# Optimization experiments

Hardware: AMD Instinct MI355X
Metric: run time of the kernel (lower is better)

The kernel has to match this reference:

```python
import jax, jax.numpy as jnp
import numpy as np

B, S, HID, NH = 8, 384, 512, 8
HD = HID // NH
SCALE = float(np.sqrt(HID))  # torch code scales by sqrt(full hidden_units), not head dim
EPS = 1e-6


def setup_inputs() -> dict:
    key = jax.random.key(0)
    ks = jax.random.split(key, 6)
    enc = jax.random.normal(ks[0], (B, S, HID), jnp.float32)
    # mask: (B,1,S,S); fill=ones, made causal (lower-triangular) so masking is exercised
    mask = jnp.broadcast_to(jnp.tril(jnp.ones((S, S), jnp.int32)), (B, 1, S, S))
    init = 1.0 / np.sqrt(HID)
    Wq = jax.random.normal(ks[1], (HID, HID), jnp.float32) * init
    Wk = jax.random.normal(ks[2], (HID, HID), jnp.float32) * init
    Wv = jax.random.normal(ks[3], (HID, HID), jnp.float32) * init
    Wo = jax.random.normal(ks[4], (HID, HID), jnp.float32) * init
    ln_gamma = jnp.ones((HID,), jnp.float32)
    ln_beta = jnp.zeros((HID,), jnp.float32)
    return {"enc": enc, "mask": mask, "Wq": Wq, "Wk": Wk, "Wv": Wv, "Wo": Wo,
            "ln_gamma": ln_gamma, "ln_beta": ln_beta}


def reference(enc, mask, Wq, Wk, Wv, Wo, ln_gamma, ln_beta):
    # enc: (B,S,HID); torch Linear(no bias): y = x @ W.T
    def heads(x, W):
        return (x @ W.T).reshape(B, S, NH, HD).transpose(0, 2, 1, 3)  # (B,H,S,D)

    q, k, v = heads(enc, Wq), heads(enc, Wk), heads(enc, Wv)
    # intersample scores: query (b,h,q) vs key (c,h,k) -> (B,H,C,Sq,Sk)
    scores = jnp.einsum('bhqd,chkd->bhcqk', q, k) / SCALE
    m = mask[:, 0]  # (C,S,S): key-sample mask
    scores = jnp.where(m[None, None] == 0, -1.0e9, scores)
    # joint softmax over (key-sample c, key-position k)
    sw = scores.transpose(0, 1, 3, 2, 4).reshape(B, NH, S, B * S)
    w = jax.nn.softmax(sw, axis=-1).reshape(B, NH, S, B, S).transpose(0, 1, 3, 2, 4)  # (B,H,C,Sq,Sk)
    ctx = jnp.einsum('bhcqk,chkd->bhqd', w, v)            # (B,H,S,D)
    ctx = ctx.transpose(0, 2, 1, 3).reshape(B, S, HID)     # (B,S,HID)
    out = ctx @ Wo.T + enc                                 # W_O + residual (dropout=identity, eval)
    mu = out.mean(-1, keepdims=True)
    var = ((out - mu) ** 2).mean(-1, keepdims=True)
    out = (out - mu) / jnp.sqrt(var + EPS) * ln_gamma + ln_beta
    return (out, w)
```

## Files before the change

kernel.cpp:

```cpp
#include <hip/hip_runtime.h>
#include <hip/hip_bf16.h>

#define B_    8
#define S_    384
#define HID_  512
#define NH_   8
#define HD_   64
#define T_    3072
static constexpr float INV_SCALE = 0.044194173824159216f;

typedef float  f32x4  __attribute__((ext_vector_type(4)));
typedef __bf16 bf16x8 __attribute__((ext_vector_type(8)));
typedef __bf16 bf16x4 __attribute__((ext_vector_type(4)));

#define MFMA(a, b, c) __builtin_amdgcn_mfma_f32_16x16x32_bf16((a), (b), (c), 0, 0, 0)

__global__ __launch_bounds__(256)
void cvt_kernel(const float* __restrict__ enc, const float* __restrict__ Wq,
                const float* __restrict__ Wk,  const float* __restrict__ Wv,
                const float* __restrict__ Wo,
                __bf16* __restrict__ encB, __bf16* __restrict__ WqB,
                __bf16* __restrict__ WkB,  __bf16* __restrict__ WvB,
                __bf16* __restrict__ WoB)
{
    const int E  = T_ * HID_ / 4;
    const int W4 = HID_ * HID_ / 4;
    int i = blockIdx.x * 256 + threadIdx.x;
    const float* src; __bf16* dst; int off;
    if      (i < E)          { src = enc; dst = encB; off = i; }
    else if (i < E + W4)     { src = Wq;  dst = WqB;  off = i - E; }
    else if (i < E + 2 * W4) { src = Wk;  dst = WkB;  off = i - E - W4; }
    else if (i < E + 3 * W4) { src = Wv;  dst = WvB;  off = i - E - 2 * W4; }
    else                     { src = Wo;  dst = WoB;  off = i - E - 3 * W4; }
    f32x4 v = *(const f32x4*)(src + (size_t)off * 4);
    bf16x4 o;
    #pragma unroll
    for (int j = 0; j < 4; ++j) o[j] = (__bf16)v[j];
    *(bf16x4*)(dst + (size_t)off * 4) = o;
}

__global__ __launch_bounds__(256)
void qkv_kernel(const __bf16* __restrict__ enc,
                const __bf16* __restrict__ Wq,
                const __bf16* __restrict__ Wk,
                const __bf16* __restrict__ Wv,
                __bf16* __restrict__ Qs,
                __bf16* __restrict__ Ks,
                __bf16* __restrict__ Vt)
{
    const int w    = threadIdx.x >> 6;
    const int lane = threadIdx.x & 63;
    const int col  = lane & 15;
    const int quad = lane >> 4;
    const int m0   = blockIdx.x * 64 + w * 16;
    const int n0   = blockIdx.y * 64;
    const int z    = blockIdx.z;
    const __bf16* W = (z == 0) ? Wq : (z == 1) ? Wk : Wv;

    f32x4 acc[4];
    #pragma unroll
    for (int j = 0; j < 4; ++j) acc[j] = (f32x4){0.f, 0.f, 0.f, 0.f};

    const __bf16* arow = enc + (size_t)(m0 + col) * HID_;
    for (int k0 = 0; k0 < HID_; k0 += 32) {
        bf16x8 a = *(const bf16x8*)(arow + k0 + quad * 8);
        #pragma unroll
        for (int j = 0; j < 4; ++j) {
            bf16x8 b = *(const bf16x8*)(W + (size_t)(n0 + j * 16 + col) * HID_ + k0 + quad * 8);
            acc[j] = MFMA(a, b, acc[j]);
        }
    }

    if (z == 2) {
        #pragma unroll
        for (int j = 0; j < 4; ++j) {
            int n = n0 + j * 16 + col;
            bf16x4 pk;
            #pragma unroll
            for (int r = 0; r < 4; ++r) pk[r] = (__bf16)acc[j][r];
            *(bf16x4*)(Vt + (size_t)n * T_ + m0 + quad * 4) = pk;
        }
    } else {
        __bf16* Oo = (z == 0) ? Qs : Ks;
        float sc = (z == 0) ? INV_SCALE : 1.0f;
        #pragma unroll
        for (int j = 0; j < 4; ++j)
            #pragma unroll
            for (int r = 0; r < 4; ++r)
                Oo[(size_t)(m0 + quad * 4 + r) * HID_ + n0 + j * 16 + col] =
                    (__bf16)(acc[j][r] * sc);
    }
}

__global__ __launch_bounds__(512)
void attn_core(const __bf16* __restrict__ Qs,
               const __bf16* __restrict__ Ks,
               const __bf16* __restrict__ Vt,
               __bf16* __restrict__ ctxB,
               float* __restrict__ rlws)
{
    const int qt   = blockIdx.x;
    const int h    = blockIdx.y;
    const int b    = blockIdx.z;
    const int tid  = threadIdx.x;
    const int W    = tid >> 6;
    const int half = W >> 2;
    const int w    = W & 3;
    const int lane = tid & 63;
    const int col  = lane & 15;
    const int quad = lane >> 4;

    __shared__ __bf16 elds[8][16][72];
    __shared__ float  cred[4][16][68];
    __shared__ float  lred[4][16][16];

    const int qq_base = w * 16 + quad * 4;

    const __bf16* qrow = Qs + (size_t)(b * S_ + qt * 64 + w * 16 + col) * HID_ + h * HD_;
    bf16x8 aQ0 = *(const bf16x8*)(qrow + quad * 8);
    bf16x8 aQ1 = *(const bf16x8*)(qrow + 32 + quad * 8);

    f32x4 acc[4];
    #pragma unroll
    for (int j = 0; j < 4; ++j) acc[j] = (f32x4){0.f, 0.f, 0.f, 0.f};
    float lp[4] = {0.f, 0.f, 0.f, 0.f};

    const int NC = B_ * (qt + 1);
    for (int idx = half; idx < NC; idx += 2) {
        const int c  = idx / (qt + 1);
        const int kc = idx % (qt + 1);
        const int kt0 = c * S_ + kc * 64;
        const bool diag = (kc == qt);
        #pragma unroll
        for (int nt = 0; nt < 4; ++nt) {
            const __bf16* krow = Ks + (size_t)(kt0 + nt * 16 + col) * HID_ + h * HD_;
            bf16x8 bK0 = *(const bf16x8*)(krow + quad * 8);
            bf16x8 bK1 = *(const bf16x8*)(krow + 32 + quad * 8);
            f32x4 s = (f32x4){0.f, 0.f, 0.f, 0.f};
            s = MFMA(aQ0, bK0, s);
            s = MFMA(aQ1, bK1, s);
            const int kk = nt * 16 + col;
            #pragma unroll
            for (int r = 0; r < 4; ++r) {
                float e = (!diag || kk <= qq_base + r) ? __expf(s[r]) : 0.f;
                lp[r] += e;
                elds[W][quad * 4 + r][kk] = (__bf16)e;
            }
        }
        #pragma unroll
        for (int ks = 0; ks < 2; ++ks) {
            bf16x8 aE = *(const bf16x8*)(&elds[W][col][ks * 32 + quad * 8]);
            #pragma unroll
            for (int nt = 0; nt < 4; ++nt) {
                bf16x8 bV = *(const bf16x8*)(Vt + (size_t)(h * HD_ + nt * 16 + col) * T_ +
                                             kt0 + ks * 32 + quad * 8);
                acc[nt] = MFMA(aE, bV, acc[nt]);
            }
        }
    }

    if (half == 1) {
        #pragma unroll
        for (int nt = 0; nt < 4; ++nt)
            #pragma unroll
            for (int r = 0; r < 4; ++r)
                cred[w][quad * 4 + r][nt * 16 + col] = acc[nt][r];
        #pragma unroll
        for (int r = 0; r < 4; ++r)
            lred[w][quad * 4 + r][col] = lp[r];
    }
    __syncthreads();
    if (half == 1) return;

    #pragma unroll
    for (int r = 0; r < 4; ++r)
        lp[r] += lred[w][quad * 4 + r][col];
    #pragma unroll
    for (int nt = 0; nt < 4; ++nt)
        #pragma unroll
        for (int r = 0; r < 4; ++r)
            acc[nt][r] += cred[w][quad * 4 + r][nt * 16 + col];

    float rl[4];
    #pragma unroll
    for (int r = 0; r < 4; ++r) {
        float v = lp[r];
        v += __shfl_xor(v, 1);
        v += __shfl_xor(v, 2);
        v += __shfl_xor(v, 4);
        v += __shfl_xor(v, 8);
        rl[r] = 1.0f / v;
    }
    if (col == 0) {
        #pragma unroll
        for (int r = 0; r < 4; ++r)
            rlws[(size_t)(b * NH_ + h) * S_ + qt * 64 + qq_base + r] = rl[r];
    }

    #pragma unroll
    for (int nt = 0; nt < 4; ++nt)
        #pragma unroll
        for (int r = 0; r < 4; ++r)
            ctxB[(size_t)(b * S_ + qt * 64 + qq_base + r) * HID_ + h * HD_ + nt * 16 + col] =
                (__bf16)(acc[nt][r] * rl[r]);
}

__global__ __launch_bounds__(256)
void tail_kernel(const __bf16* __restrict__ Qs,
                 const __bf16* __restrict__ Ks,
                 const float* __restrict__ rlws,
                 float* __restrict__ wout,
                 const __bf16* __restrict__ ctxB,
                 const __bf16* __restrict__ WoB,
                 const float* __restrict__ enc,
                 const float* __restrict__ gamma,
                 const float* __restrict__ beta,
                 float* __restrict__ out)
{
    const int tid  = threadIdx.x;
    const int w    = tid >> 6;
    const int lane = tid & 63;
    const int col  = lane & 15;
    const int quad = lane >> 4;

    __shared__ float elds[4][16][68];
    __shared__ float s_sums[16][4][2];

    if (blockIdx.x < 3) {
        const int t0 = ((blockIdx.x * NH_ + blockIdx.y) * B_ + blockIdx.z) * 16;
        const int wv = w;

        f32x4 acc[8];
        #pragma unroll
        for (int nt = 0; nt < 8; ++nt) acc[nt] = (f32x4){0.f, 0.f, 0.f, 0.f};

        const __bf16* arow = ctxB + (size_t)(t0 + col) * HID_;
        for (int step = 0; step < 16; ++step) {
            bf16x8 a = *(const bf16x8*)(arow + step * 32 + quad * 8);
            #pragma unroll
            for (int nt = 0; nt < 8; ++nt) {
                bf16x8 bW = *(const bf16x8*)(WoB + (size_t)(wv * 128 + nt * 16 + col) * HID_ +
                                             step * 32 + quad * 8);
                acc[nt] = MFMA(a, bW, acc[nt]);
            }
        }

        const int trow = t0 + quad * 4;
        float psum[4] = {0.f, 0.f, 0.f, 0.f};
        float psq[4]  = {0.f, 0.f, 0.f, 0.f};
        #pragma unroll
        for (int nt = 0; nt < 8; ++nt) {
            int n = wv * 128 + nt * 16 + col;
            #pragma unroll
            for (int r = 0; r < 4; ++r) {
                float x = acc[nt][r] + enc[(size_t)(trow + r) * HID_ + n];
                acc[nt][r] = x;
                psum[r] += x;
                psq[r]  += x * x;
            }
        }
        #pragma unroll
        for (int r = 0; r < 4; ++r) {
            float v = psum[r], q2 = psq[r];
            v  += __shfl_xor(v, 1);  v  += __shfl_xor(v, 2);
            v  += __shfl_xor(v, 4);  v  += __shfl_xor(v, 8);
            q2 += __shfl_xor(q2, 1); q2 += __shfl_xor(q2, 2);
            q2 += __shfl_xor(q2, 4); q2 += __shfl_xor(q2, 8);
            if (col == 0) {
                s_sums[quad * 4 + r][wv][0] = v;
                s_sums[quad * 4 + r][wv][1] = q2;
            }
        }
        __syncthreads();

        #pragma unroll
        for (int r = 0; r < 4; ++r) {
            float sm = s_sums[quad * 4 + r][0][0] + s_sums[quad * 4 + r][1][0] +
                       s_sums[quad * 4 + r][2][0] + s_sums[quad * 4 + r][3][0];
            float sq = s_sums[quad * 4 + r][0][1] + s_sums[quad * 4 + r][1][1] +
                       s_sums[quad * 4 + r][2][1] + s_sums[quad * 4 + r][3][1];
            float mu   = sm * (1.0f / 512.0f);
            float var  = sq * (1.0f / 512.0f) - mu * mu;
            float rstd = rsqrtf(var + 1e-6f);
            #pragma unroll
            for (int nt = 0; nt < 8; ++nt) {
                int n = wv * 128 + nt * 16 + col;
                float y = (acc[nt][r] - mu) * rstd * gamma[n] + beta[n];
                out[(size_t)(trow + r) * HID_ + n] = y;
            }
        }
        return;
    }

    const int x    = blockIdx.x - 3;
    const int qt   = x % 6;
    const int c    = x / 6;
    const int h    = blockIdx.y;
    const int b    = blockIdx.z;
    const int wr   = lane >> 2;
    const int seg  = lane & 3;

    const int qq_base = w * 16 + quad * 4;

    const __bf16* qrow = Qs + (size_t)(b * S_ + qt * 64 + w * 16 + col) * HID_ + h * HD_;
    bf16x8 aQ0 = *(const bf16x8*)(qrow + quad * 8);
    bf16x8 aQ1 = *(const bf16x8*)(qrow + 32 + quad * 8);

    float rlv[4];
    #pragma unroll
    for (int r = 0; r < 4; ++r)
        rlv[r] = rlws[(size_t)(b * NH_ + h) * S_ + qt * 64 + qq_base + r];

    float* gb = wout + ((((size_t)(b * NH_ + h) * B_ + c) * S_ + qt * 64 + w * 16 + wr) * S_);

    for (int kc = 0; kc < 6; ++kc) {
        float* gp = gb + kc * 64 + seg * 16;
        if (kc > qt) {
            #pragma unroll
            for (int j = 0; j < 4; ++j)
                *(f32x4*)(gp + j * 4) = (f32x4){0.f, 0.f, 0.f, 0.f};
            continue;
        }
        const int kt0 = c * S_ + kc * 64;
        const bool diag = (kc == qt);
        #pragma unroll
        for (int nt = 0; nt < 4; ++nt) {
            const __bf16* krow = Ks + (size_t)(kt0 + nt * 16 + col) * HID_ + h * HD_;
            bf16x8 bK0 = *(const bf16x8*)(krow + quad * 8);
            bf16x8 bK1 = *(const bf16x8*)(krow + 32 + quad * 8);
            f32x4 s = (f32x4){0.f, 0.f, 0.f, 0.f};
            s = MFMA(aQ0, bK0, s);
            s = MFMA(aQ1, bK1, s);
            const int kk = nt * 16 + col;
            #pragma unroll
            for (int r = 0; r < 4; ++r) {
                float e = (!diag || kk <= qq_base + r) ? __expf(s[r]) * rlv[r] : 0.f;
                elds[w][quad * 4 + r][kk] = e;
            }
        }
        #pragma unroll
        for (int j = 0; j < 4; ++j)
            *(f32x4*)(gp + j * 4) = *(const f32x4*)(&elds[w][wr][seg * 16 + j * 4]);
    }
}

extern "C" void kernel_launch(void* const* d_in, const int* in_sizes, int n_in,
                              void* d_out, int out_size, void* d_ws, size_t ws_size,
                              hipStream_t stream)
{
    const float* enc   = (const float*)d_in[0];
    const float* Wq    = (const float*)d_in[2];
    const float* Wk    = (const float*)d_in[3];
    const float* Wv    = (const float*)d_in[4];
    const float* Wo    = (const float*)d_in[5];
    const float* gamma = (const float*)d_in[6];
    const float* beta  = (const float*)d_in[7];

    float* out  = (float*)d_out;
    float* wout = out + (size_t)T_ * HID_;

    char* ws = (char*)d_ws;
    const size_t SZ_TOK = (size_t)T_ * HID_ * sizeof(__bf16);
    const size_t SZ_W   = (size_t)HID_ * HID_ * sizeof(__bf16);
    __bf16* encB = (__bf16*)(ws);
    __bf16* WqB  = (__bf16*)(ws + SZ_TOK);
    __bf16* WkB  = (__bf16*)(ws + SZ_TOK + SZ_W);
    __bf16* WvB  = (__bf16*)(ws + SZ_TOK + 2 * SZ_W);
    __bf16* WoB  = (__bf16*)(ws + SZ_TOK + 3 * SZ_W);
    __bf16* Qs   = (__bf16*)(ws + SZ_TOK + 4 * SZ_W);
    __bf16* Ks   = (__bf16*)(ws + 2 * SZ_TOK + 4 * SZ_W);
    __bf16* Vt   = (__bf16*)(ws + 3 * SZ_TOK + 4 * SZ_W);
    __bf16* ctxB = (__bf16*)(ws + 4 * SZ_TOK + 4 * SZ_W);
    float*  rlws = (float*)(ws);

    cvt_kernel<<<dim3(2560), 256, 0, stream>>>(enc, Wq, Wk, Wv, Wo,
                                               encB, WqB, WkB, WvB, WoB);
    qkv_kernel<<<dim3(48, 8, 3), 256, 0, stream>>>(encB, WqB, WkB, WvB, Qs, Ks, Vt);
    attn_core<<<dim3(6, NH_, B_), 512, 0, stream>>>(Qs, Ks, Vt, ctxB, rlws);
    tail_kernel<<<dim3(51, NH_, B_), 256, 0, stream>>>(Qs, Ks, rlws, wout,
                                                       ctxB, WoB, enc, gamma, beta, out);
}
```

Baseline: 601.7 us.

## Fuse all stages into one cooperative persistent kernel with grid syncs

Merges the conversion, QKV projection, attention core and tail (weights output plus output projection and layernorm) into a single cooperative kernel of 256 blocks, with grid-wide syncs between stages. Work units are distributed over the persistent blocks in strided loops. This removes the gaps between kernel launches and the launch overhead, at the cost of grid-sync latency and a fixed block count that may balance poorly across stages. The original multi-kernel path stays as a fallback when cooperative launch is unavailable.

```diff
diff --git a/kernel.cpp b/kernel.cpp
--- a/kernel.cpp
+++ b/kernel.cpp
@@ -1,5 +1,8 @@
 #include <hip/hip_runtime.h>
+#include <hip/hip_cooperative_groups.h>
 #include <hip/hip_bf16.h>
+
+namespace cg = cooperative_groups;
 
 #define B_    8
 #define S_    384
@@ -14,6 +17,347 @@
 typedef __bf16 bf16x4 __attribute__((ext_vector_type(4)));
 
 #define MFMA(a, b, c) __builtin_amdgcn_mfma_f32_16x16x32_bf16((a), (b), (c), 0, 0, 0)
+
+#define NBLK 256
+#define NTHR 512
+
+__global__ __launch_bounds__(512, 2)
+void mega_kernel(const float* __restrict__ enc,
+                 const float* __restrict__ Wq,  const float* __restrict__ Wk,
+                 const float* __restrict__ Wv,  const float* __restrict__ Wo,
+                 const float* __restrict__ gamma, const float* __restrict__ beta,
+                 __bf16* __restrict__ encB, __bf16* __restrict__ WqB,
+                 __bf16* __restrict__ WkB,  __bf16* __restrict__ WvB,
+                 __bf16* __restrict__ WoB,
+                 __bf16* __restrict__ Qs,   __bf16* __restrict__ Ks,
+                 __bf16* __restrict__ Vt,   __bf16* __restrict__ ctxB,
+                 float* __restrict__ rlws,  float* __restrict__ wout,
+                 float* __restrict__ out)
+{
+    cg::grid_group grid = cg::this_grid();
+    const int blk = blockIdx.x;
+    const int tid = threadIdx.x;
+
+    __shared__ __align__(16) char smem[39936];
+
+    {
+        const int E  = T_ * HID_ / 4;
+        const int W4 = HID_ * HID_ / 4;
+        const int TOT = E + 4 * W4;
+        for (int i = blk * NTHR + tid; i < TOT; i += NBLK * NTHR) {
+            const float* src; __bf16* dst; int off;
+            if      (i < E)          { src = enc; dst = encB; off = i; }
+            else if (i < E + W4)     { src = Wq;  dst = WqB;  off = i - E; }
+            else if (i < E + 2 * W4) { src = Wk;  dst = WkB;  off = i - E - W4; }
+            else if (i < E + 3 * W4) { src = Wv;  dst = WvB;  off = i - E - 2 * W4; }
+            else                     { src = Wo;  dst = WoB;  off = i - E - 3 * W4; }
+            f32x4 v = *(const f32x4*)(src + (size_t)off * 4);
+            bf16x4 o;
+            #pragma unroll
+            for (int j = 0; j < 4; ++j) o[j] = (__bf16)v[j];
+            *(bf16x4*)(dst + (size_t)off * 4) = o;
+        }
+    }
+    grid.sync();
+
+    {
+        const int half = tid >> 8;
+        const int t2   = tid & 255;
+        const int w    = t2 >> 6;
+        const int lane = t2 & 63;
+        const int col  = lane & 15;
+        const int quad = lane >> 4;
+        for (int u = blk; u < 576; u += NBLK) {
+            const int vb = u * 2 + half;
+            const int x  = vb % 48;
+            const int y  = (vb / 48) % 8;
+            const int z  = vb / 384;
+            const int m0 = x * 64 + w * 16;
+            const int n0 = y * 64;
+            const __bf16* W = (z == 0) ? WqB : (z == 1) ? WkB : WvB;
+
+            f32x4 acc[4];
+            #pragma unroll
+            for (int j = 0; j < 4; ++j) acc[j] = (f32x4){0.f, 0.f, 0.f, 0.f};
+
+            const __bf16* arow = encB + (size_t)(m0 + col) * HID_;
+            for (int k0 = 0; k0 < HID_; k0 += 32) {
+                bf16x8 a = *(const bf16x8*)(arow + k0 + quad * 8);
+                #pragma unroll
+                for (int j = 0; j < 4; ++j) {
+                    bf16x8 b = *(const bf16x8*)(W + (size_t)(n0 + j * 16 + col) * HID_ + k0 + quad * 8);
+                    acc[j] = MFMA(a, b, acc[j]);
+                }
+            }
+
+            if (z == 2) {
+                #pragma unroll
+                for (int j = 0; j < 4; ++j) {
+                    int n = n0 + j * 16 + col;
+                    bf16x4 pk;
+                    #pragma unroll
+                    for (int r = 0; r < 4; ++r) pk[r] = (__bf16)acc[j][r];
+                    *(bf16x4*)(Vt + (size_t)n * T_ + m0 + quad * 4) = pk;
+                }
+            } else {
+                __bf16* Oo = (z == 0) ? Qs : Ks;
+                float sc = (z == 0) ? INV_SCALE : 1.0f;
+                #pragma unroll
+                for (int j = 0; j < 4; ++j)
+                    #pragma unroll
+                    for (int r = 0; r < 4; ++r)
+                        Oo[(size_t)(m0 + quad * 4 + r) * HID_ + n0 + j * 16 + col] =
+                            (__bf16)(acc[j][r] * sc);
+            }
+        }
+    }
+    grid.sync();
+
+    {
+        const int W    = tid >> 6;
+        const int half = W >> 2;
+        const int w    = W & 3;
+        const int lane = tid & 63;
+        const int col  = lane & 15;
+        const int quad = lane >> 4;
+
+        __bf16 (*elds)[16][72] = (__bf16(*)[16][72])(smem);
+        float  (*cred)[16][68] = (float(*)[16][68])(smem + 18432);
+        float  (*lred)[16][16] = (float(*)[16][16])(smem + 35840);
+
+        const int qq_base = w * 16 + quad * 4;
+
+        for (int u = blk; u < 384; u += NBLK) {
+            const int qt = u % 6;
+            const int h  = (u / 6) % 8;
+            const int b  = u / 48;
+
+            const __bf16* qrow = Qs + (size_t)(b * S_ + qt * 64 + w * 16 + col) * HID_ + h * HD_;
+            bf16x8 aQ0 = *(const bf16x8*)(qrow + quad * 8);
+            bf16x8 aQ1 = *(const bf16x8*)(qrow + 32 + quad * 8);
+
+            f32x4 acc[4];
+            #pragma unroll
+            for (int j = 0; j < 4; ++j) acc[j] = (f32x4){0.f, 0.f, 0.f, 0.f};
+            float lp[4] = {0.f, 0.f, 0.f, 0.f};
+
+            const int NC = B_ * (qt + 1);
+            for (int idx = half; idx < NC; idx += 2) {
+                const int c  = idx / (qt + 1);
+                const int kc = idx % (qt + 1);
+                const int kt0 = c * S_ + kc * 64;
+                const bool diag = (kc == qt);
+                #pragma unroll
+                for (int nt = 0; nt < 4; ++nt) {
+                    const __bf16* krow = Ks + (size_t)(kt0 + nt * 16 + col) * HID_ + h * HD_;
+                    bf16x8 bK0 = *(const bf16x8*)(krow + quad * 8);
+                    bf16x8 bK1 = *(const bf16x8*)(krow + 32 + quad * 8);
+                    f32x4 s = (f32x4){0.f, 0.f, 0.f, 0.f};
+                    s = MFMA(aQ0, bK0, s);
+                    s = MFMA(aQ1, bK1, s);
+                    const int kk = nt * 16 + col;
+                    #pragma unroll
+                    for (int r = 0; r < 4; ++r) {
+                        float e = (!diag || kk <= qq_base + r) ? __expf(s[r]) : 0.f;
+                        lp[r] += e;
+                        elds[W][quad * 4 + r][kk] = (__bf16)e;
+                    }
+                }
+                #pragma unroll
+                for (int ks = 0; ks < 2; ++ks) {
+                    bf16x8 aE = *(const bf16x8*)(&elds[W][col][ks * 32 + quad * 8]);
+                    #pragma unroll
+                    for (int nt = 0; nt < 4; ++nt) {
+                        bf16x8 bV = *(const bf16x8*)(Vt + (size_t)(h * HD_ + nt * 16 + col) * T_ +
+                                                     kt0 + ks * 32 + quad * 8);
+                        acc[nt] = MFMA(aE, bV, acc[nt]);
+                    }
+                }
+            }
+
+            if (half == 1) {
+                #pragma unroll
+                for (int nt = 0; nt < 4; ++nt)
+                    #pragma unroll
+                    for (int r = 0; r < 4; ++r)
+                        cred[w][quad * 4 + r][nt * 16 + col] = acc[nt][r];
+                #pragma unroll
+                for (int r = 0; r < 4; ++r)
+                    lred[w][quad * 4 + r][col] = lp[r];
+            }
+            __syncthreads();
+            if (half == 0) {
+                #pragma unroll
+                for (int r = 0; r < 4; ++r)
+                    lp[r] += lred[w][quad * 4 + r][col];
+                #pragma unroll
+                for (int nt = 0; nt < 4; ++nt)
+                    #pragma unroll
+                    for (int r = 0; r < 4; ++r)
+                        acc[nt][r] += cred[w][quad * 4 + r][nt * 16 + col];
+
+                float rl[4];
+                #pragma unroll
+                for (int r = 0; r < 4; ++r) {
+                    float v = lp[r];
+                    v += __shfl_xor(v, 1);
+                    v += __shfl_xor(v, 2);
+                    v += __shfl_xor(v, 4);
+                    v += __shfl_xor(v, 8);
+                    rl[r] = 1.0f / v;
+                }
+                if (col == 0) {
+                    #pragma unroll
+                    for (int r = 0; r < 4; ++r)
+                        rlws[(size_t)(b * NH_ + h) * S_ + qt * 64 + qq_base + r] = rl[r];
+                }
+                #pragma unroll
+                for (int nt = 0; nt < 4; ++nt)
+                    #pragma unroll
+                    for (int r = 0; r < 4; ++r)
+                        ctxB[(size_t)(b * S_ + qt * 64 + qq_base + r) * HID_ + h * HD_ + nt * 16 + col] =
+                            (__bf16)(acc[nt][r] * rl[r]);
+            }
+            __syncthreads();
+        }
+    }
+    grid.sync();
+
+    {
+        for (int u = blk; u < 1728; u += NBLK) {
+            if (u < 192) {
+                const int t0   = u * 16;
+                const int wv   = tid >> 6;
+                const int lane = tid & 63;
+                const int col  = lane & 15;
+                const int quad = lane >> 4;
+                float (*s_sums)[8][2] = (float(*)[8][2])(smem + 34816);
+
+                f32x4 acc[4];
+                #pragma unroll
+                for (int nt = 0; nt < 4; ++nt) acc[nt] = (f32x4){0.f, 0.f, 0.f, 0.f};
+
+                const __bf16* arow = ctxB + (size_t)(t0 + col) * HID_;
+                for (int step = 0; step < 16; ++step) {
+                    bf16x8 a = *(const bf16x8*)(arow + step * 32 + quad * 8);
+                    #pragma unroll
+                    for (int nt = 0; nt < 4; ++nt) {
+                        bf16x8 bW = *(const bf16x8*)(WoB + (size_t)(wv * 64 + nt * 16 + col) * HID_ +
+                                                     step * 32 + quad * 8);
+                        acc[nt] = MFMA(a, bW, acc[nt]);
+                    }
+                }
+
+                const int trow = t0 + quad * 4;
+                float psum[4] = {0.f, 0.f, 0.f, 0.f};
+                float psq[4]  = {0.f, 0.f, 0.f, 0.f};
+                #pragma unroll
+                for (int nt = 0; nt < 4; ++nt) {
+                    int n = wv * 64 + nt * 16 + col;
+                    #pragma unroll
+                    for (int r = 0; r < 4; ++r) {
+                        float x = acc[nt][r] + enc[(size_t)(trow + r) * HID_ + n];
+                        acc[nt][r] = x;
+                        psum[r] += x;
+                        psq[r]  += x * x;
+                    }
+                }
+                #pragma unroll
+                for (int r = 0; r < 4; ++r) {
+                    float v = psum[r], q2 = psq[r];
+                    v  += __shfl_xor(v, 1);  v  += __shfl_xor(v, 2);
+                    v  += __shfl_xor(v, 4);  v  += __shfl_xor(v, 8);
+                    q2 += __shfl_xor(q2, 1); q2 += __shfl_xor(q2, 2);
+                    q2 += __shfl_xor(q2, 4); q2 += __shfl_xor(q2, 8);
+                    if (col == 0) {
+                        s_sums[quad * 4 + r][wv][0] = v;
+                        s_sums[quad * 4 + r][wv][1] = q2;
+                    }
+                }
+                __syncthreads();
+
+                #pragma unroll
+                for (int r = 0; r < 4; ++r) {
+                    float sm = 0.f, sq = 0.f;
+                    #pragma unroll
+                    for (int q = 0; q < 8; ++q) {
+                        sm += s_sums[quad * 4 + r][q][0];
+                        sq += s_sums[quad * 4 + r][q][1];
+                    }
+                    float mu   = sm * (1.0f / 512.0f);
+                    float var  = sq * (1.0f / 512.0f) - mu * mu;
+                    float rstd = rsqrtf(var + 1e-6f);
+                    #pragma unroll
+                    for (int nt = 0; nt < 4; ++nt) {
+                        int n = wv * 64 + nt * 16 + col;
+                        float y = (acc[nt][r] - mu) * rstd * gamma[n] + beta[n];
+                        out[(size_t)(trow + r) * HID_ + n] = y;
+                    }
+                }
+                __syncthreads();
+            } else {
+                const int half = tid >> 8;
+                const int t2   = tid & 255;
+                const int vb   = (u - 192) * 2 + half;
+                const int x    = vb % 48;
+                const int qt   = x % 6;
+                const int c    = x / 6;
+                const int h    = (vb / 48) % 8;
+                const int b    = vb / 384;
+                const int w    = t2 >> 6;
+                const int lane = t2 & 63;
+                const int col  = lane & 15;
+                const int quad = lane >> 4;
+                const int wr   = lane >> 2;
+                const int seg  = lane & 3;
+                float (*elds)[16][68] = (float(*)[16][68])(smem + half * 17408);
+
+                const int qq_base = w * 16 + quad * 4;
+
+                const __bf16* qrow = Qs + (size_t)(b * S_ + qt * 64 + w * 16 + col) * HID_ + h * HD_;
+                bf16x8 aQ0 = *(const bf16x8*)(qrow + quad * 8);
+                bf16x8 aQ1 = *(const bf16x8*)(qrow + 32 + quad * 8);
+
+                float rlv[4];
+                #pragma unroll
+                for (int r = 0; r < 4; ++r)
+                    rlv[r] = rlws[(size_t)(b * NH_ + h) * S_ + qt * 64 + qq_base + r];
+
+                float* gb = wout + ((((size_t)(b * NH_ + h) * B_ + c) * S_ + qt * 64 + w * 16 + wr) * S_);
+
+                for (int kc = 0; kc < 6; ++kc) {
+                    float* gp = gb + kc * 64 + seg * 16;
+                    if (kc > qt) {
+                        #pragma unroll
+                        for (int j = 0; j < 4; ++j)
+                            *(f32x4*)(gp + j * 4) = (f32x4){0.f, 0.f, 0.f, 0.f};
+                        continue;
+                    }
+                    const int kt0 = c * S_ + kc * 64;
+                    const bool diag = (kc == qt);
+                    #pragma unroll
+                    for (int nt = 0; nt < 4; ++nt) {
+                        const __bf16* krow = Ks + (size_t)(kt0 + nt * 16 + col) * HID_ + h * HD_;
+                        bf16x8 bK0 = *(const bf16x8*)(krow + quad * 8);
+                        bf16x8 bK1 = *(const bf16x8*)(krow + 32 + quad * 8);
+                        f32x4 s = (f32x4){0.f, 0.f, 0.f, 0.f};
+                        s = MFMA(aQ0, bK0, s);
+                        s = MFMA(aQ1, bK1, s);
+                        const int kk = nt * 16 + col;
+                        #pragma unroll
+                        for (int r = 0; r < 4; ++r) {
+                            float e = (!diag || kk <= qq_base + r) ? __expf(s[r]) * rlv[r] : 0.f;
+                            elds[w][quad * 4 + r][kk] = e;
+                        }
+                    }
+                    #pragma unroll
+                    for (int j = 0; j < 4; ++j)
+                        *(f32x4*)(gp + j * 4) = *(const f32x4*)(&elds[w][wr][seg * 16 + j * 4]);
+                }
+            }
+        }
+    }
+}
 
 __global__ __launch_bounds__(256)
 void cvt_kernel(const float* __restrict__ enc, const float* __restrict__ Wq,
@@ -196,7 +540,6 @@
         for (int r = 0; r < 4; ++r)
             rlws[(size_t)(b * NH_ + h) * S_ + qt * 64 + qq_base + r] = rl[r];
     }
-
     #pragma unroll
     for (int nt = 0; nt < 4; ++nt)
         #pragma unroll
@@ -373,10 +716,40 @@
     __bf16* ctxB = (__bf16*)(ws + 4 * SZ_TOK + 4 * SZ_W);
     float*  rlws = (float*)(ws);
 
-    cvt_kernel<<<dim3(2560), 256, 0, stream>>>(enc, Wq, Wk, Wv, Wo,
-                                               encB, WqB, WkB, WvB, WoB);
-    qkv_kernel<<<dim3(48, 8, 3), 256, 0, stream>>>(encB, WqB, WkB, WvB, Qs, Ks, Vt);
-    attn_core<<<dim3(6, NH_, B_), 512, 0, stream>>>(Qs, Ks, Vt, ctxB, rlws);
-    tail_kernel<<<dim3(51, NH_, B_), 256, 0, stream>>>(Qs, Ks, rlws, wout,
-                                                       ctxB, WoB, enc, gamma, beta, out);
+    static int coop_ok = -1;
+    if (coop_ok < 0) {
+        int dev = 0;
+        (void)hipGetDevice(&dev);
+        int attr = 0;
+        (void)hipDeviceGetAttribute(&attr, hipDeviceAttributeCooperativeLaunch, dev);
+        int occ = 0;
+        (void)hipOccupancyMaxActiveBlocksPerMultiprocessor(&occ, mega_kernel, NTHR, 0);
+        int nCU = 0;
+        (void)hipDeviceGetAttribute(&nCU, hipDeviceAttributeMultiprocessorCount, dev);
+        coop_ok = (attr != 0 && occ >= 1 && (long)occ * nCU >= NBLK) ? 1 : 0;
+    }
+
+    bool done = false;
+    if (coop_ok == 1) {
+        void* args[] = {
+            (void*)&enc, (void*)&Wq, (void*)&Wk, (void*)&Wv, (void*)&Wo,
+            (void*)&gamma, (void*)&beta,
+            (void*)&encB, (void*)&WqB, (void*)&WkB, (void*)&WvB, (void*)&WoB,
+            (void*)&Qs, (void*)&Ks, (void*)&Vt, (void*)&ctxB,
+            (void*)&rlws, (void*)&wout, (void*)&out
+        };
+        hipError_t e = hipLaunchCooperativeKernel((void*)mega_kernel, dim3(NBLK),
+                                                  dim3(NTHR), args, 0, stream);
+        if (e == hipSuccess) done = true;
+        else coop_ok = 0;
+    }
+
+    if (!done) {
+        cvt_kernel<<<dim3(2560), 256, 0, stream>>>(enc, Wq, Wk, Wv, Wo,
+                                                   encB, WqB, WkB, WvB, WoB);
+        qkv_kernel<<<dim3(48, 8, 3), 256, 0, stream>>>(encB, WqB, WkB, WvB, Qs, Ks, Vt);
+        attn_core<<<dim3(6, NH_, B_), 512, 0, stream>>>(Qs, Ks, Vt, ctxB, rlws);
+        tail_kernel<<<dim3(51, NH_, B_), 256, 0, stream>>>(Qs, Ks, rlws, wout,
+                                                           ctxB, WoB, enc, gamma, beta, out);
+    }
 }
```

After: 601.3 us. About the same (-0.1%).

## Fuse conversion, projection and attention into a cooperative kernel, store unnormalized probs

Applied to the files above, without the earlier changes.

Merges the cast, QKV projection and attention stages into one cooperative persistent kernel, with grid-wide syncs between stages, to cut launch gaps and tail effects. Attention now writes the unnormalized exponentials (bf16 scratch or fp32 directly into the output) while it computes them. The tail kernel then only rescales by the row reciprocal instead of recomputing QK^T and exp. This trades recomputation for extra scratch traffic: the bf16 buffer is large, and the fp32 fallback does a read-modify-write of the weight output. It also relies on cooperative-launch support being available, falling back to separate kernels otherwise.

```diff
diff --git a/kernel.cpp b/kernel.cpp
--- a/kernel.cpp
+++ b/kernel.cpp
@@ -1,5 +1,8 @@
 #include <hip/hip_runtime.h>
+#include <hip/hip_cooperative_groups.h>
 #include <hip/hip_bf16.h>
+
+namespace cg = cooperative_groups;
 
 #define B_    8
 #define S_    384
@@ -15,17 +18,20 @@
 
 #define MFMA(a, b, c) __builtin_amdgcn_mfma_f32_16x16x32_bf16((a), (b), (c), 0, 0, 0)
 
-__global__ __launch_bounds__(256)
-void cvt_kernel(const float* __restrict__ enc, const float* __restrict__ Wq,
-                const float* __restrict__ Wk,  const float* __restrict__ Wv,
-                const float* __restrict__ Wo,
-                __bf16* __restrict__ encB, __bf16* __restrict__ WqB,
-                __bf16* __restrict__ WkB,  __bf16* __restrict__ WvB,
-                __bf16* __restrict__ WoB)
+#define NBLK 256
+#define NTHR 512
+
+
+__device__ __forceinline__ void cvt_unit(int i,
+    const float* __restrict__ enc, const float* __restrict__ Wq,
+    const float* __restrict__ Wk,  const float* __restrict__ Wv,
+    const float* __restrict__ Wo,
+    __bf16* __restrict__ encB, __bf16* __restrict__ WqB,
+    __bf16* __restrict__ WkB,  __bf16* __restrict__ WvB,
+    __bf16* __restrict__ WoB)
 {
     const int E  = T_ * HID_ / 4;
     const int W4 = HID_ * HID_ / 4;
-    int i = blockIdx.x * 256 + threadIdx.x;
     const float* src; __bf16* dst; int off;
     if      (i < E)          { src = enc; dst = encB; off = i; }
     else if (i < E + W4)     { src = Wq;  dst = WqB;  off = i - E; }
@@ -39,29 +45,27 @@
     *(bf16x4*)(dst + (size_t)off * 4) = o;
 }
 
-__global__ __launch_bounds__(256)
-void qkv_kernel(const __bf16* __restrict__ enc,
-                const __bf16* __restrict__ Wq,
-                const __bf16* __restrict__ Wk,
-                const __bf16* __restrict__ Wv,
-                __bf16* __restrict__ Qs,
-                __bf16* __restrict__ Ks,
-                __bf16* __restrict__ Vt)
-{
-    const int w    = threadIdx.x >> 6;
-    const int lane = threadIdx.x & 63;
+__device__ __forceinline__ void qkv_unit(int vb, int t2,
+    const __bf16* __restrict__ encB, const __bf16* __restrict__ WqB,
+    const __bf16* __restrict__ WkB,  const __bf16* __restrict__ WvB,
+    __bf16* __restrict__ Qs, __bf16* __restrict__ Ks, __bf16* __restrict__ Vt)
+{
+    const int w    = t2 >> 6;
+    const int lane = t2 & 63;
     const int col  = lane & 15;
     const int quad = lane >> 4;
-    const int m0   = blockIdx.x * 64 + w * 16;
-    const int n0   = blockIdx.y * 64;
-    const int z    = blockIdx.z;
-    const __bf16* W = (z == 0) ? Wq : (z == 1) ? Wk : Wv;
+    const int x  = vb % 48;
+    const int y  = (vb / 48) % 8;
+    const int z  = vb / 384;
+    const int m0 = x * 64 + w * 16;
+    const int n0 = y * 64;
+    const __bf16* W = (z == 0) ? WqB : (z == 1) ? WkB : WvB;
 
     f32x4 acc[4];
     #pragma unroll
     for (int j = 0; j < 4; ++j) acc[j] = (f32x4){0.f, 0.f, 0.f, 0.f};
 
-    const __bf16* arow = enc + (size_t)(m0 + col) * HID_;
+    const __bf16* arow = encB + (size_t)(m0 + col) * HID_;
     for (int k0 = 0; k0 < HID_; k0 += 32) {
         bf16x8 a = *(const bf16x8*)(arow + k0 + quad * 8);
         #pragma unroll
@@ -92,17 +96,15 @@
     }
 }
 
-__global__ __launch_bounds__(512)
-void attn_core(const __bf16* __restrict__ Qs,
-               const __bf16* __restrict__ Ks,
-               const __bf16* __restrict__ Vt,
-               __bf16* __restrict__ ctxB,
-               float* __restrict__ rlws)
-{
-    const int qt   = blockIdx.x;
-    const int h    = blockIdx.y;
-    const int b    = blockIdx.z;
-    const int tid  = threadIdx.x;
+__device__ __forceinline__ void attn_unit(int u, int tid, char* smem,
+    const __bf16* __restrict__ Qs, const __bf16* __restrict__ Ks,
+    const __bf16* __restrict__ Vt, __bf16* __restrict__ ctxB,
+    float* __restrict__ rlws, __bf16* __restrict__ eB,
+    float* __restrict__ wout, int useBf16)
+{
+    const int qt   = u % 6;
+    const int h    = (u / 6) % 8;
+    const int b    = u / 48;
     const int W    = tid >> 6;
     const int half = W >> 2;
     const int w    = W & 3;
@@ -110,9 +112,9 @@
     const int col  = lane & 15;
     const int quad = lane >> 4;
 
-    __shared__ __bf16 elds[8][16][72];
-    __shared__ float  cred[4][16][68];
-    __shared__ float  lred[4][16][16];
+    __bf16 (*elds)[16][72] = (__bf16(*)[16][72])(smem);
+    float  (*cred)[16][68] = (float(*)[16][68])(smem + 18432);
+    float  (*lred)[16][16] = (float(*)[16][16])(smem + 35840);
 
     const int qq_base = w * 16 + quad * 4;
 
@@ -124,6 +126,10 @@
     #pragma unroll
     for (int j = 0; j < 4; ++j) acc[j] = (f32x4){0.f, 0.f, 0.f, 0.f};
     float lp[4] = {0.f, 0.f, 0.f, 0.f};
+
+    const size_t qg   = (size_t)(b * NH_ + h) * S_ + qt * 64 + w * 16 + col;
+    __bf16* ebase = eB + qg * T_;
+    float*  wbase = wout + (((size_t)(b * NH_ + h) * B_) * S_ + qt * 64 + w * 16 + col) * S_;
 
     const int NC = B_ * (qt + 1);
     for (int idx = half; idx < NC; idx += 2) {
@@ -150,6 +156,16 @@
         #pragma unroll
         for (int ks = 0; ks < 2; ++ks) {
             bf16x8 aE = *(const bf16x8*)(&elds[W][col][ks * 32 + quad * 8]);
+            if (useBf16) {
+                *(bf16x8*)(ebase + c * S_ + kc * 64 + ks * 32 + quad * 8) = aE;
+            } else {
+                float* wp = wbase + (size_t)c * S_ * S_ + kc * 64 + ks * 32 + quad * 8;
+                f32x4 lo, hi;
+                #pragma unroll
+                for (int j = 0; j < 4; ++j) { lo[j] = (float)aE[j]; hi[j] = (float)aE[j + 4]; }
+                *(f32x4*)wp = lo;
+                *(f32x4*)(wp + 4) = hi;
+            }
             #pragma unroll
             for (int nt = 0; nt < 4; ++nt) {
                 bf16x8 bV = *(const bf16x8*)(Vt + (size_t)(h * HD_ + nt * 16 + col) * T_ +
@@ -170,64 +186,121 @@
             lred[w][quad * 4 + r][col] = lp[r];
     }
     __syncthreads();
-    if (half == 1) return;
-
-    #pragma unroll
-    for (int r = 0; r < 4; ++r)
-        lp[r] += lred[w][quad * 4 + r][col];
-    #pragma unroll
-    for (int nt = 0; nt < 4; ++nt)
+    if (half == 0) {
         #pragma unroll
         for (int r = 0; r < 4; ++r)
-            acc[nt][r] += cred[w][quad * 4 + r][nt * 16 + col];
-
-    float rl[4];
-    #pragma unroll
-    for (int r = 0; r < 4; ++r) {
-        float v = lp[r];
-        v += __shfl_xor(v, 1);
-        v += __shfl_xor(v, 2);
-        v += __shfl_xor(v, 4);
-        v += __shfl_xor(v, 8);
-        rl[r] = 1.0f / v;
-    }
-    if (col == 0) {
-        #pragma unroll
-        for (int r = 0; r < 4; ++r)
-            rlws[(size_t)(b * NH_ + h) * S_ + qt * 64 + qq_base + r] = rl[r];
-    }
-
-    #pragma unroll
-    for (int nt = 0; nt < 4; ++nt)
-        #pragma unroll
-        for (int r = 0; r < 4; ++r)
-            ctxB[(size_t)(b * S_ + qt * 64 + qq_base + r) * HID_ + h * HD_ + nt * 16 + col] =
-                (__bf16)(acc[nt][r] * rl[r]);
+            lp[r] += lred[w][quad * 4 + r][col];
+        #pragma unroll
+        for (int nt = 0; nt < 4; ++nt)
+            #pragma unroll
+            for (int r = 0; r < 4; ++r)
+                acc[nt][r] += cred[w][quad * 4 + r][nt * 16 + col];
+
+        float rl[4];
+        #pragma unroll
+        for (int r = 0; r < 4; ++r) {
+            float v = lp[r];
+            v += __shfl_xor(v, 1);
+            v += __shfl_xor(v, 2);
+            v += __shfl_xor(v, 4);
+            v += __shfl_xor(v, 8);
+            rl[r] = 1.0f / v;
+        }
+        if (col == 0) {
+            #pragma unroll
+            for (int r = 0; r < 4; ++r)
+                rlws[(size_t)(b * NH_ + h) * S_ + qt * 64 + qq_base + r] = rl[r];
+        }
+        #pragma unroll
+        for (int nt = 0; nt < 4; ++nt)
+            #pragma unroll
+            for (int r = 0; r < 4; ++r)
+                ctxB[(size_t)(b * S_ + qt * 64 + qq_base + r) * HID_ + h * HD_ + nt * 16 + col] =
+                    (__bf16)(acc[nt][r] * rl[r]);
+    }
+}
+
+__global__ __launch_bounds__(512, 2)
+void mega1(const float* __restrict__ enc,
+           const float* __restrict__ Wq,  const float* __restrict__ Wk,
+           const float* __restrict__ Wv,  const float* __restrict__ Wo,
+           __bf16* __restrict__ encB, __bf16* __restrict__ WqB,
+           __bf16* __restrict__ WkB,  __bf16* __restrict__ WvB,
+           __bf16* __restrict__ WoB,
+           __bf16* __restrict__ Qs,   __bf16* __restrict__ Ks,
+           __bf16* __restrict__ Vt,   __bf16* __restrict__ ctxB,
+           float* __restrict__ rlws,  __bf16* __restrict__ eB,
+           float* __restrict__ wout,  int useBf16)
+{
+    cg::grid_group grid = cg::this_grid();
+    const int blk = blockIdx.x;
+    const int tid = threadIdx.x;
+
+    __shared__ __align__(16) char smem[39936];
+
+    {
+        const int TOT = T_ * HID_ / 4 + HID_ * HID_;
+        for (int i = blk * NTHR + tid; i < TOT; i += NBLK * NTHR)
+            cvt_unit(i, enc, Wq, Wk, Wv, Wo, encB, WqB, WkB, WvB, WoB);
+    }
+    grid.sync();
+
+    {
+        const int half = tid >> 8;
+        const int t2   = tid & 255;
+        for (int u = blk; u < 576; u += NBLK)
+            qkv_unit(u * 2 + half, t2, encB, WqB, WkB, WvB, Qs, Ks, Vt);
+    }
+    grid.sync();
+
+    for (int u = blk; u < 384; u += NBLK) {
+        attn_unit(u, tid, smem, Qs, Ks, Vt, ctxB, rlws, eB, wout, useBf16);
+        __syncthreads();
+    }
 }
 
 __global__ __launch_bounds__(256)
-void tail_kernel(const __bf16* __restrict__ Qs,
-                 const __bf16* __restrict__ Ks,
-                 const float* __restrict__ rlws,
-                 float* __restrict__ wout,
-                 const __bf16* __restrict__ ctxB,
-                 const __bf16* __restrict__ WoB,
-                 const float* __restrict__ enc,
-                 const float* __restrict__ gamma,
-                 const float* __restrict__ beta,
-                 float* __restrict__ out)
-{
-    const int tid  = threadIdx.x;
-    const int w    = tid >> 6;
-    const int lane = tid & 63;
-    const int col  = lane & 15;
-    const int quad = lane >> 4;
-
-    __shared__ float elds[4][16][68];
-    __shared__ float s_sums[16][4][2];
-
-    if (blockIdx.x < 3) {
-        const int t0 = ((blockIdx.x * NH_ + blockIdx.y) * B_ + blockIdx.z) * 16;
+void cvt_kernel(const float* enc, const float* Wq, const float* Wk,
+                const float* Wv, const float* Wo,
+                __bf16* encB, __bf16* WqB, __bf16* WkB, __bf16* WvB, __bf16* WoB)
+{
+    int i = blockIdx.x * 256 + threadIdx.x;
+    cvt_unit(i, enc, Wq, Wk, Wv, Wo, encB, WqB, WkB, WvB, WoB);
+}
+
+__global__ __launch_bounds__(256)
+void qkv_kernel(const __bf16* encB, const __bf16* WqB, const __bf16* WkB,
+                const __bf16* WvB, __bf16* Qs, __bf16* Ks, __bf16* Vt)
+{
+    int vb = blockIdx.x + 48 * (blockIdx.y + 8 * blockIdx.z);
+    qkv_unit(vb, threadIdx.x, encB, WqB, WkB, WvB, Qs, Ks, Vt);
+}
+
+__global__ __launch_bounds__(512)
+void attn_sep(const __bf16* Qs, const __bf16* Ks, const __bf16* Vt,
+              __bf16* ctxB, float* rlws, __bf16* eB, float* wout, int useBf16)
+{
+    __shared__ __align__(16) char smem[39936];
+    attn_unit(blockIdx.x, threadIdx.x, smem, Qs, Ks, Vt, ctxB, rlws, eB, wout, useBf16);
+}
+
+__global__ __launch_bounds__(256)
+void tail2(const float* __restrict__ rlws, const __bf16* __restrict__ eB,
+           const __bf16* __restrict__ ctxB, const __bf16* __restrict__ WoB,
+           const float* __restrict__ enc, const float* __restrict__ gamma,
+           const float* __restrict__ beta, float* __restrict__ wout,
+           float* __restrict__ out, int useBf16)
+{
+    const int tid = threadIdx.x;
+
+    if (blockIdx.x < 192) {
+        const int w    = tid >> 6;
+        const int lane = tid & 63;
+        const int col  = lane & 15;
+        const int quad = lane >> 4;
+        __shared__ float s_sums[16][4][2];
+
+        const int t0 = blockIdx.x * 16;
         const int wv = w;
 
         f32x4 acc[8];
@@ -292,55 +365,37 @@
         return;
     }
 
-    const int x    = blockIdx.x - 3;
-    const int qt   = x % 6;
-    const int c    = x / 6;
-    const int h    = blockIdx.y;
-    const int b    = blockIdx.z;
-    const int wr   = lane >> 2;
-    const int seg  = lane & 3;
-
-    const int qq_base = w * 16 + quad * 4;
-
-    const __bf16* qrow = Qs + (size_t)(b * S_ + qt * 64 + w * 16 + col) * HID_ + h * HD_;
-    bf16x8 aQ0 = *(const bf16x8*)(qrow + quad * 8);
-    bf16x8 aQ1 = *(const bf16x8*)(qrow + 32 + quad * 8);
-
-    float rlv[4];
-    #pragma unroll
-    for (int r = 0; r < 4; ++r)
-        rlv[r] = rlws[(size_t)(b * NH_ + h) * S_ + qt * 64 + qq_base + r];
-
-    float* gb = wout + ((((size_t)(b * NH_ + h) * B_ + c) * S_ + qt * 64 + w * 16 + wr) * S_);
-
-    for (int kc = 0; kc < 6; ++kc) {
-        float* gp = gb + kc * 64 + seg * 16;
-        if (kc > qt) {
-            #pragma unroll
-            for (int j = 0; j < 4; ++j)
-                *(f32x4*)(gp + j * 4) = (f32x4){0.f, 0.f, 0.f, 0.f};
-            continue;
-        }
-        const int kt0 = c * S_ + kc * 64;
-        const bool diag = (kc == qt);
-        #pragma unroll
-        for (int nt = 0; nt < 4; ++nt) {
-            const __bf16* krow = Ks + (size_t)(kt0 + nt * 16 + col) * HID_ + h * HD_;
-            bf16x8 bK0 = *(const bf16x8*)(krow + quad * 8);
-            bf16x8 bK1 = *(const bf16x8*)(krow + 32 + quad * 8);
-            f32x4 s = (f32x4){0.f, 0.f, 0.f, 0.f};
-            s = MFMA(aQ0, bK0, s);
-            s = MFMA(aQ1, bK1, s);
-            const int kk = nt * 16 + col;
-            #pragma unroll
-            for (int r = 0; r < 4; ++r) {
-                float e = (!diag || kk <= qq_base + r) ? __expf(s[r]) * rlv[r] : 0.f;
-                elds[w][quad * 4 + r][kk] = e;
-            }
-        }
-        #pragma unroll
-        for (int j = 0; j < 4; ++j)
-            *(f32x4*)(gp + j * 4) = *(const f32x4*)(&elds[w][wr][seg * 16 + j * 4]);
+    const int u  = blockIdx.x - 192;
+    const int bh = u >> 3;
+    const int c  = u & 7;
+    float* wbase = wout + ((size_t)bh * B_ + c) * S_ * S_;
+    const __bf16* ebase = eB + (size_t)bh * S_ * T_ + c * S_;
+    const float* rlbase = rlws + (size_t)bh * S_;
+
+    const int NCHUNK = S_ * (S_ / 8);
+    for (int idx = tid; idx < NCHUNK; idx += 256) {
+        const int q  = idx / 48;
+        const int k8 = (idx - q * 48) * 8;
+        float* wp = wbase + (size_t)q * S_ + k8;
+        if ((k8 >> 6) > (q >> 6)) {
+            *(f32x4*)wp       = (f32x4){0.f, 0.f, 0.f, 0.f};
+            *(f32x4*)(wp + 4) = (f32x4){0.f, 0.f, 0.f, 0.f};
+        } else {
+            const float rl = rlbase[q];
+            f32x4 lo, hi;
+            if (useBf16) {
+                bf16x8 e = *(const bf16x8*)(ebase + (size_t)q * T_ + k8);
+                #pragma unroll
+                for (int j = 0; j < 4; ++j) { lo[j] = (float)e[j] * rl; hi[j] = (float)e[j + 4] * rl; }
+            } else {
+                f32x4 e0 = *(const f32x4*)wp;
+                f32x4 e1 = *(const f32x4*)(wp + 4);
+                #pragma unroll
+                for (int j = 0; j < 4; ++j) { lo[j] = e0[j] * rl; hi[j] = e1[j] * rl; }
+            }
+            *(f32x4*)wp       = lo;
+            *(f32x4*)(wp + 4) = hi;
+        }
     }
 }
 
@@ -373,10 +428,44 @@
     __bf16* ctxB = (__bf16*)(ws + 4 * SZ_TOK + 4 * SZ_W);
     float*  rlws = (float*)(ws);
 
-    cvt_kernel<<<dim3(2560), 256, 0, stream>>>(enc, Wq, Wk, Wv, Wo,
-                                               encB, WqB, WkB, WvB, WoB);
-    qkv_kernel<<<dim3(48, 8, 3), 256, 0, stream>>>(encB, WqB, WkB, WvB, Qs, Ks, Vt);
-    attn_core<<<dim3(6, NH_, B_), 512, 0, stream>>>(Qs, Ks, Vt, ctxB, rlws);
-    tail_kernel<<<dim3(51, NH_, B_), 256, 0, stream>>>(Qs, Ks, rlws, wout,
-                                                       ctxB, WoB, enc, gamma, beta, out);
-}
+    const size_t BASE   = 5 * SZ_TOK + 4 * SZ_W;
+    const size_t SZ_EB  = (size_t)(B_ * NH_) * S_ * T_ * sizeof(__bf16);
+    int useBf16 = (ws_size >= BASE + SZ_EB) ? 1 : 0;
+    __bf16* eB = (__bf16*)(ws + BASE);
+
+    static int coop_ok = -1;
+    if (coop_ok < 0) {
+        int dev = 0;
+        (void)hipGetDevice(&dev);
+        int attr = 0;
+        (void)hipDeviceGetAttribute(&attr, hipDeviceAttributeCooperativeLaunch, dev);
+        int occ = 0;
+        (void)hipOccupancyMaxActiveBlocksPerMultiprocessor(&occ, mega1, NTHR, 0);
+        int nCU = 0;
+        (void)hipDeviceGetAttribute(&nCU, hipDeviceAttributeMultiprocessorCount, dev);
+        coop_ok = (attr != 0 && occ >= 1 && (long)occ * nCU >= NBLK) ? 1 : 0;
+    }
+
+    bool done = false;
+    if (coop_ok == 1) {
+        void* args[] = {
+            (void*)&enc, (void*)&Wq, (void*)&Wk, (void*)&Wv, (void*)&Wo,
+            (void*)&encB, (void*)&WqB, (void*)&WkB, (void*)&WvB, (void*)&WoB,
+            (void*)&Qs, (void*)&Ks, (void*)&Vt, (void*)&ctxB,
+            (void*)&rlws, (void*)&eB, (void*)&wout, (void*)&useBf16
+        };
+        hipError_t e = hipLaunchCooperativeKernel((void*)mega1, dim3(NBLK),
+                                                  dim3(NTHR), args, 0, stream);
+        if (e == hipSuccess) done = true;
+        else coop_ok = 0;
+    }
+    if (!done) {
+        cvt_kernel<<<dim3(2560), 256, 0, stream>>>(enc, Wq, Wk, Wv, Wo,
+                                                   encB, WqB, WkB, WvB, WoB);
+        qkv_kernel<<<dim3(48, 8, 3), 256, 0, stream>>>(encB, WqB, WkB, WvB, Qs, Ks, Vt);
+        attn_sep<<<dim3(384), 512, 0, stream>>>(Qs, Ks, Vt, ctxB, rlws, eB, wout, useBf16);
+    }
+
+    tail2<<<dim3(192 + 512), 256, 0, stream>>>(rlws, eB, ctxB, WoB, enc,
+                                               gamma, beta, wout, out, useBf16);
+}
```

Result: slower. 665.7 us (+10.6%).
